# Optimization experiments

Measured on AMD Instinct MI355X. Metric: run time of the kernel, lower is better.

Reference implementation:

```python
import jax, jax.numpy as jnp
import numpy as np

N = 4096      # num_nodes (unbatched seq len for the transformer)
D = 128       # input_dim = window = d_model
H = 4         # num_heads
DH = D // H
DFF = 2048    # PyTorch TransformerEncoderLayer default dim_feedforward
HID = 256     # hidden_dim
OUT = 64      # output_dim
E = 131072    # num_edges (avg degree 32)
EPS = 1e-5    # LayerNorm eps (torch default)


def layer_norm(x, g, b):
    mu = jnp.mean(x, axis=-1, keepdims=True)
    var = jnp.var(x, axis=-1, keepdims=True)
    return (x - mu) * jax.lax.rsqrt(var + EPS) * g + b


def gcn_conv(x, W, b, src, dst):
    # PyG GCNConv: h = x W^T; add self-loops; symmetric deg^-1/2 norm; scatter-add at dst; + bias
    h = x @ W.T
    loop = jnp.arange(N)
    s = jnp.concatenate([src, loop])
    t = jnp.concatenate([dst, loop])
    deg = jax.ops.segment_sum(jnp.ones_like(t, dtype=h.dtype), t, num_segments=N)
    dinv = jnp.where(deg > 0, jax.lax.rsqrt(jnp.maximum(deg, 1e-12)), 0.0)
    norm = dinv[s] * dinv[t]                                   # [E+N]
    out = jax.ops.segment_sum(h[s] * norm[:, None], t, num_segments=N)
    return out + b


def setup_inputs() -> dict:
    key = jax.random.key(0)
    ks = jax.random.split(key, 12)
    sc = 0.05
    w = lambda k, shape: jax.random.normal(k, shape, dtype=jnp.float32) * sc
    return {
        "x": jax.random.normal(ks[0], (N, D), dtype=jnp.float32),
        "edge_index": jax.random.randint(ks[1], (2, E), 0, N),
        "in_proj_w": w(ks[2], (3 * D, D)),
        "in_proj_b": jnp.zeros((3 * D,), jnp.float32),
        "out_proj_w": w(ks[3], (D, D)),
        "out_proj_b": jnp.zeros((D,), jnp.float32),
        "ln1_g": jnp.ones((D,), jnp.float32),
        "ln1_b": jnp.zeros((D,), jnp.float32),
        "ffn_w1": w(ks[4], (DFF, D)),
        "ffn_b1": jnp.zeros((DFF,), jnp.float32),
        "ffn_w2": w(ks[5], (D, DFF)),
        "ffn_b2": jnp.zeros((D,), jnp.float32),
        "ln2_g": jnp.ones((D,), jnp.float32),
        "ln2_b": jnp.zeros((D,), jnp.float32),
        "gcn1_w": w(ks[6], (HID, D)),
        "gcn1_b": jnp.zeros((HID,), jnp.float32),
        "gcn2_w": w(ks[7], (HID, HID)),
        "gcn2_b": jnp.zeros((HID,), jnp.float32),
        "gcn3_w": w(ks[8], (OUT, HID)),
        "gcn3_b": jnp.zeros((OUT,), jnp.float32),
    }


def reference(x, edge_index, in_proj_w, in_proj_b, out_proj_w, out_proj_b,
              ln1_g, ln1_b, ffn_w1, ffn_b1, ffn_w2, ffn_b2, ln2_g, ln2_b,
              gcn1_w, gcn1_b, gcn2_w, gcn2_b, gcn3_w, gcn3_b):
    src, dst = edge_index[0], edge_index[1]
    # --- TransformerEncoderLayer (post-norm, relu, dropout=0, unbatched [N, D]) ---
    qkv = x @ in_proj_w.T + in_proj_b
    q, k, v = jnp.split(qkv, 3, axis=-1)
    q = q.reshape(N, H, DH)
    k = k.reshape(N, H, DH)
    v = v.reshape(N, H, DH)
    scores = jnp.einsum('nhd,mhd->hnm', q, k) / jnp.sqrt(jnp.float32(DH))
    attn = jax.nn.softmax(scores, axis=-1)
    ctx = jnp.einsum('hnm,mhd->nhd', attn, v).reshape(N, D)
    attn_out = ctx @ out_proj_w.T + out_proj_b
    y = layer_norm(x + attn_out, ln1_g, ln1_b)
    ff = jax.nn.relu(y @ ffn_w1.T + ffn_b1) @ ffn_w2.T + ffn_b2
    z = layer_norm(y + ff, ln2_g, ln2_b)
    # x.squeeze(-1) is a no-op since window (=128) > 1
    # --- 3-layer GCN with ReLU between layers ---
    h = jax.nn.relu(gcn_conv(z, gcn1_w, gcn1_b, src, dst))
    h = jax.nn.relu(gcn_conv(h, gcn2_w, gcn2_b, src, dst))
    return gcn_conv(h, gcn3_w, gcn3_b, src, dst)
```

## Files before the change

kernel.cpp:

```cpp
#include <hip/hip_runtime.h>


typedef unsigned short u16;
typedef __attribute__((ext_vector_type(8))) short bf16x8;
typedef __attribute__((ext_vector_type(4))) float f32x4;

__device__ __forceinline__ float b2f(u16 u) {
  union { unsigned int i; float f; } x; x.i = ((unsigned int)u) << 16; return x.f;
}
__device__ __forceinline__ u16 f2b(float f) {
  union { float f; unsigned int i; } x; x.f = f;
  unsigned int r = x.i + 0x7FFFu + ((x.i >> 16) & 1u);
  return (u16)(r >> 16);
}
__device__ __forceinline__ float ld1(const void* p, size_t i, int bf) {
  return bf ? b2f(((const u16*)p)[i]) : ((const float*)p)[i];
}

__device__ void gemm_body(
    int bx, int by, int bz, int nz,
    const void* __restrict__ A, const void* __restrict__ B,
    const void* __restrict__ bias, void* __restrict__ C, void* __restrict__ C2,
    int N, int K, int lda, int ldb, int bRow0, int bK0, int flags,
    const int* __restrict__ dflag, const float* __restrict__ divL)
{
  const int wbf = *dflag;
  const int abf = (flags & 64) ? 0 : ((flags & 16) ? wbf : 1);
  __shared__ u16 As[64][128];
  __shared__ u16 Bs[64][128];
  const int tid = threadIdx.x;
  const int wv = tid >> 6, l = tid & 63;
  const int lr = l & 15, lq = l >> 4;
  const int row0 = by * 64, col0 = bx * 64;
  const int qr = 32 * (wv >> 1), qc = 32 * (wv & 1);
  const int sr = tid >> 2, sb = tid & 3;
  const int Kz = K / nz;
  const int k0 = bz * Kz;
  f32x4 acc[2][2] = {};
  for (int kt = k0; kt < k0 + Kz; kt += 128) {
    __syncthreads();
#pragma unroll
    for (int g = 0; g < 4; g++) {
      int b = sb + 4 * g;
      int cc = b * 8;
      int bs = (b ^ (sr & 15)) * 8;
      size_t offA = (size_t)(row0 + sr) * lda + kt + cc;
      if (abf) {
        *(bf16x8*)&As[sr][bs] = *(const bf16x8*)((const u16*)A + offA);
      } else {
        const float* pf = (const float*)A + offA;
        float iv = divL
            ? 1.0f / divL[(size_t)((kt + cc) >> 5) * 4096 + row0 + sr]
            : 1.0f;
        float4 f0 = *(const float4*)pf, f1 = *(const float4*)(pf + 4);
        u16 t[8] = {f2b(f0.x*iv), f2b(f0.y*iv), f2b(f0.z*iv), f2b(f0.w*iv),
                    f2b(f1.x*iv), f2b(f1.y*iv), f2b(f1.z*iv), f2b(f1.w*iv)};
        *(bf16x8*)&As[sr][bs] = *(bf16x8*)t;
      }
      size_t offB = (size_t)(bRow0 + col0 + sr) * ldb + bK0 + kt + cc;
      if (wbf) {
        *(bf16x8*)&Bs[sr][bs] = *(const bf16x8*)((const u16*)B + offB);
      } else {
        const float* pf = (const float*)B + offB;
        float4 f0 = *(const float4*)pf, f1 = *(const float4*)(pf + 4);
        u16 t[8] = {f2b(f0.x), f2b(f0.y), f2b(f0.z), f2b(f0.w),
                    f2b(f1.x), f2b(f1.y), f2b(f1.z), f2b(f1.w)};
        *(bf16x8*)&Bs[sr][bs] = *(bf16x8*)t;
      }
    }
    __syncthreads();
#pragma unroll
    for (int kk = 0; kk < 4; kk++) {
      int bxs = ((4 * kk + lq) ^ lr) * 8;
      bf16x8 a0 = *(const bf16x8*)&As[qr + lr][bxs];
      bf16x8 a1 = *(const bf16x8*)&As[qr + 16 + lr][bxs];
      bf16x8 b0 = *(const bf16x8*)&Bs[qc + lr][bxs];
      bf16x8 b1 = *(const bf16x8*)&Bs[qc + 16 + lr][bxs];
      acc[0][0] = __builtin_amdgcn_mfma_f32_16x16x32_bf16(a0, b0, acc[0][0], 0, 0, 0);
      acc[0][1] = __builtin_amdgcn_mfma_f32_16x16x32_bf16(a0, b1, acc[0][1], 0, 0, 0);
      acc[1][0] = __builtin_amdgcn_mfma_f32_16x16x32_bf16(a1, b0, acc[1][0], 0, 0, 0);
      acc[1][1] = __builtin_amdgcn_mfma_f32_16x16x32_bf16(a1, b1, acc[1][1], 0, 0, 0);
    }
  }
  if ((flags & 128) && col0 >= 256) {
#pragma unroll
    for (int i = 0; i < 2; i++) {
#pragma unroll
      for (int j = 0; j < 2; j++) {
        int colg = col0 + qc + 16 * j + lr;
        int d = colg - 256;
        int rowbase = row0 + qr + 16 * i + lq * 4;
        float bb = ld1(bias, colg, wbf);
        ushort4 pv = make_ushort4(
            f2b(acc[i][j][0] + bb), f2b(acc[i][j][1] + bb),
            f2b(acc[i][j][2] + bb), f2b(acc[i][j][3] + bb));
        *(ushort4*)((u16*)C2 + (size_t)d * 4096 + rowbase) = pv;
      }
    }
    return;
  }
  const int ldc = (flags & 128) ? 256 : N;
#pragma unroll
  for (int i = 0; i < 2; i++) {
#pragma unroll
    for (int j = 0; j < 2; j++) {
#pragma unroll
      for (int r = 0; r < 4; r++) {
        int row = row0 + qr + 16 * i + lq * 4 + r;
        int col = col0 + qc + 16 * j + lr;
        float v = acc[i][j][r];
        if (flags & 8) v += ld1(bias, bRow0 + col, wbf);
        if (flags & 1) v = fmaxf(v, 0.f);
        size_t idx = (size_t)row * ldc + col;
        if (flags & 32) {
          atomicAdd(&((float*)C)[idx], v);
        } else if (flags & 4) {
          float* Cf = (float*)C;
          if (flags & 2) v += Cf[idx];
          Cf[idx] = v;
        } else {
          ((u16*)C)[idx] = f2b(v);
        }
      }
    }
  }
}

__global__ __launch_bounds__(256) void gemm_mfma(
    const void* __restrict__ A, const void* __restrict__ B,
    const void* __restrict__ bias, void* __restrict__ C, void* __restrict__ C2,
    int N, int K, int lda, int ldb, int bRow0, int bK0, int flags,
    const int* __restrict__ dflag, const float* __restrict__ divL)
{
  gemm_body(blockIdx.x, blockIdx.y, blockIdx.z, gridDim.z,
            A, B, bias, C, C2, N, K, lda, ldb, bRow0, bK0, flags, dflag, divL);
}

__global__ __launch_bounds__(256) void det_count(
    const void* __restrict__ x, int* __restrict__ flag,
    const int* __restrict__ dst, int* __restrict__ counts, int E)
{
  if (blockIdx.x == 0) {
    __shared__ int cnt;
    if (threadIdx.x == 0) cnt = 0;
    __syncthreads();
    const u16* p = (const u16*)x;
    int c = 0;
    for (int i = threadIdx.x; i < 4096; i += 256) {
      int e = (p[i] >> 7) & 0xFF;
      if (e >= 140) c++;
    }
    atomicAdd(&cnt, c);
    __syncthreads();
    if (threadIdx.x == 0) flag[0] = (cnt < 64) ? 1 : 0;
  } else {
    int e = (blockIdx.x - 1) * 256 + threadIdx.x;
    if (e < E) atomicAdd(&counts[dst[e]], 1);
  }
}

__global__ __launch_bounds__(256) void csr_inproj(
    const void* __restrict__ xin, const void* __restrict__ W,
    const void* __restrict__ bias, void* __restrict__ qkQK, void* __restrict__ Vg,
    const int* __restrict__ dflag,
    const int* __restrict__ src, const int* __restrict__ dst,
    const int* __restrict__ offs, int* __restrict__ cursor,
    int* __restrict__ csr, int E)
{
  if (blockIdx.x < 384) {
    gemm_body(blockIdx.x % 6, blockIdx.x / 6, 0, 1,
              xin, W, bias, qkQK, Vg, 384, 128, 128, 128, 0, 0,
               8 | 16 | 128, dflag, nullptr);
  } else {
    int e = (blockIdx.x - 384) * 256 + threadIdx.x;
    if (e < E) {
      int t = dst[e];
      int pos = offs[t] + atomicAdd(&cursor[t], 1);
      csr[pos] = src[e];
    }
  }
}

__global__ __launch_bounds__(256) void attn_part(
    const u16* __restrict__ qk, const u16* __restrict__ Vg,
    float* __restrict__ O, float* __restrict__ L)
{
  const int qt = blockIdx.x, h = blockIdx.y, kc = blockIdx.z;
  const int n0 = qt * 64;
  __shared__ u16 Qs[64][32];
  __shared__ u16 Ks[128][32];
  __shared__ u16 Vt[32][128];
  __shared__ u16 Ps[64][128];
  const int tid = threadIdx.x;
  const int wv = tid >> 6, l = tid & 63;
  const int lr = l & 15, lq = l >> 4;
  const int sr = tid >> 2, sb = tid & 3;
  const int kr = tid >> 1, kb = tid & 1;
  const int vr = tid >> 3, vb = tid & 7;
  *(bf16x8*)&Qs[sr][(sb ^ (sr & 3)) * 8] =
      *(const bf16x8*)(qk + (size_t)(n0 + sr) * 256 + h * 32 + sb * 8);
  __syncthreads();
  const float sc = 0.17677669529663687f;
  bf16x8 qf;
  {
    bf16x8 qraw = *(const bf16x8*)&Qs[16 * wv + lr][(lq ^ (lr & 3)) * 8];
#pragma unroll
    for (int t = 0; t < 8; t++)
      qf[t] = (short)f2b(b2f((u16)qraw[t]) * sc);
  }
  f32x4 o0 = {}, o1 = {};
  float psum[4] = {0.f, 0.f, 0.f, 0.f};
  for (int t = 0; t < 8; t++) {
    const int m0 = kc * 1024 + t * 128;
    __syncthreads();
#pragma unroll
    for (int cc = 0; cc < 2; cc++) {
      int ch = kb + 2 * cc;
      *(bf16x8*)&Ks[kr][(ch ^ (kr & 3)) * 8] =
          *(const bf16x8*)(qk + (size_t)(m0 + kr) * 256 + 128 + h * 32 + ch * 8);
    }
#pragma unroll
    for (int cc = 0; cc < 2; cc++) {
      int ch = vb + 8 * cc;
      *(bf16x8*)&Vt[vr][(ch ^ (vr & 15)) * 8] =
          *(const bf16x8*)(Vg + (size_t)(h * 32 + vr) * 4096 + m0 + ch * 8);
    }
    __syncthreads();
    f32x4 s[8];
#pragma unroll
    for (int jt = 0; jt < 8; jt++) {
      bf16x8 kf = *(const bf16x8*)&Ks[16 * jt + lr][(lq ^ (lr & 3)) * 8];
      f32x4 z = {};
      s[jt] = __builtin_amdgcn_mfma_f32_16x16x32_bf16(qf, kf, z, 0, 0, 0);
    }
#pragma unroll
    for (int jt = 0; jt < 8; jt++)
#pragma unroll
      for (int r = 0; r < 4; r++) {
        float p = __expf(s[jt][r]);
        psum[r] += p;
        int qrow = 16 * wv + lq * 4 + r;
        int ch = 2 * jt + (lr >> 3);
        Ps[qrow][(ch ^ (qrow & 15)) * 8 + (lr & 7)] = f2b(p);
      }
    __syncthreads();
#pragma unroll
    for (int kk = 0; kk < 4; kk++) {
      int prow = 16 * wv + lr;
      bf16x8 pf = *(const bf16x8*)&Ps[prow][((4 * kk + lq) ^ (lr & 15)) * 8];
      bf16x8 v0 = *(const bf16x8*)&Vt[lr][((4 * kk + lq) ^ (lr & 15)) * 8];
      bf16x8 v1 = *(const bf16x8*)&Vt[16 + lr][((4 * kk + lq) ^ (lr & 15)) * 8];
      o0 = __builtin_amdgcn_mfma_f32_16x16x32_bf16(pf, v0, o0, 0, 0, 0);
      o1 = __builtin_amdgcn_mfma_f32_16x16x32_bf16(pf, v1, o1, 0, 0, 0);
    }
  }
#pragma unroll
  for (int r = 0; r < 4; r++) {
    int row = n0 + 16 * wv + lq * 4 + r;
    atomicAdd(&O[(size_t)row * 128 + h * 32 + lr],      o0[r]);
    atomicAdd(&O[(size_t)row * 128 + h * 32 + 16 + lr], o1[r]);
    float ps = psum[r];
    ps += __shfl_xor(ps, 1); ps += __shfl_xor(ps, 2);
    ps += __shfl_xor(ps, 4); ps += __shfl_xor(ps, 8);
    if (lr == 0) atomicAdd(&L[h * 4096 + row], ps);
  }
}

__global__ __launch_bounds__(256) void ln_res(
    const void* __restrict__ A, int a_mode, const float* __restrict__ R,
    const void* __restrict__ rbias,
    const void* __restrict__ g, const void* __restrict__ b,
    u16* __restrict__ out_bf, float* __restrict__ out_f32,
    const int* __restrict__ dflag)
{
  const int wbf = *dflag;
  const int abf = a_mode ? wbf : 0;
  int row = blockIdx.x * 4 + (threadIdx.x >> 6);
  int lane = threadIdx.x & 63;
  size_t i0 = (size_t)row * 128 + lane, i1 = i0 + 64;
  float v0 = ld1(A, i0, abf) + R[i0];
  float v1 = ld1(A, i1, abf) + R[i1];
  if (rbias) { v0 += ld1(rbias, lane, wbf); v1 += ld1(rbias, lane + 64, wbf); }
  float s = v0 + v1, sq = v0 * v0 + v1 * v1;
  for (int off = 32; off; off >>= 1) { s += __shfl_down(s, off); sq += __shfl_down(sq, off); }
  s = __shfl(s, 0); sq = __shfl(sq, 0);
  float mu = s * (1.f / 128.f);
  float var = sq * (1.f / 128.f) - mu * mu;
  float rs = rsqrtf(var + 1e-5f);
  float r0 = (v0 - mu) * rs * ld1(g, lane, wbf) + ld1(b, lane, wbf);
  float r1 = (v1 - mu) * rs * ld1(g, lane + 64, wbf) + ld1(b, lane + 64, wbf);
  out_bf[i0] = f2b(r0);
  out_bf[i1] = f2b(r1);
  if (out_f32) { out_f32[i0] = r0; out_f32[i1] = r1; }
}

__global__ __launch_bounds__(1024) void scan4096(
    const int* __restrict__ counts, int* __restrict__ offs,
    float* __restrict__ dinv)
{
  __shared__ int buf[4096];
  __shared__ int part[1024];
  int t = threadIdx.x;
  for (int i = t; i < 4096; i += 1024) buf[i] = counts[i];
  __syncthreads();
  int base = t * 4;
  int s = buf[base] + buf[base + 1] + buf[base + 2] + buf[base + 3];
  part[t] = s;
  __syncthreads();
  for (int off = 1; off < 1024; off <<= 1) {
    int v = (t >= off) ? part[t - off] : 0;
    __syncthreads();
    part[t] += v;
    __syncthreads();
  }
  int run = (t == 0) ? 0 : part[t - 1];
  for (int j = 0; j < 4; j++) {
    int c = buf[base + j];
    offs[base + j] = run;
    dinv[base + j] = rsqrtf((float)(c + 1));
    run += c;
  }
  if (t == 1023) offs[4096] = run;
}

__global__ __launch_bounds__(256) void gcn_gather(
    const u16* __restrict__ h, const float* __restrict__ dinv,
    const int* __restrict__ offs, const int* __restrict__ csr,
    const void* __restrict__ bias, void* __restrict__ out,
    int F, int relu, int final_out, const int* __restrict__ dflag)
{
  const int wbf = *dflag;
  const int tpn = F >> 2;
  const int node = blockIdx.x * (256 / tpn) + threadIdx.x / tpn;
  const int f = (threadIdx.x % tpn) * 4;
  float di = dinv[node];
  ushort4 hv = *(const ushort4*)(h + (size_t)node * F + f);
  float a0 = di * b2f(hv.x), a1 = di * b2f(hv.y);
  float a2 = di * b2f(hv.z), a3 = di * b2f(hv.w);
  int e0 = offs[node], e1 = offs[node + 1];
  for (int e = e0; e < e1; e++) {
    int s = csr[e];
    float ds = dinv[s];
    ushort4 sv = *(const ushort4*)(h + (size_t)s * F + f);
    a0 += ds * b2f(sv.x); a1 += ds * b2f(sv.y);
    a2 += ds * b2f(sv.z); a3 += ds * b2f(sv.w);
  }
  float b0 = bias ? ld1(bias, f, wbf)     : 0.f;
  float b1 = bias ? ld1(bias, f + 1, wbf) : 0.f;
  float b2 = bias ? ld1(bias, f + 2, wbf) : 0.f;
  float b3 = bias ? ld1(bias, f + 3, wbf) : 0.f;
  float v0 = a0 * di + b0, v1 = a1 * di + b1;
  float v2 = a2 * di + b2, v3 = a3 * di + b3;
  if (relu) {
    v0 = fmaxf(v0, 0.f); v1 = fmaxf(v1, 0.f);
    v2 = fmaxf(v2, 0.f); v3 = fmaxf(v3, 0.f);
  }
  size_t idx = (size_t)node * F + f;
  if (!final_out || wbf) {
    *(ushort4*)((u16*)out + idx) = make_ushort4(f2b(v0), f2b(v1), f2b(v2), f2b(v3));
  } else {
    *(float4*)((float*)out + idx) = make_float4(v0, v1, v2, v3);
  }
}

extern "C" void kernel_launch(void* const* d_in, const int* in_sizes, int n_in,
                              void* d_out, int out_size, void* d_ws, size_t ws_size,
                              hipStream_t stream)
{
  const void* x          = d_in[0];
  const int*  edge       = (const int*)d_in[1];
  const void* in_proj_w  = d_in[2];
  const void* in_proj_b  = d_in[3];
  const void* out_proj_w = d_in[4];
  const void* out_proj_b = d_in[5];
  const void* ln1_g      = d_in[6];
  const void* ln1_b      = d_in[7];
  const void* ffn_w1     = d_in[8];
  const void* ffn_b1     = d_in[9];
  const void* ffn_w2     = d_in[10];
  const void* ffn_b2     = d_in[11];
  const void* ln2_g      = d_in[12];
  const void* ln2_b      = d_in[13];
  const void* g1w        = d_in[14];
  const void* g1b        = d_in[15];
  const void* g2w        = d_in[16];
  const void* g2b        = d_in[17];
  const void* g3w        = d_in[18];
  const void* g3b        = d_in[19];
  const int E = in_sizes[1] / 2;
  const int* esrc = edge;
  const int* edst = edge + E;

  char* wsb     = (char*)d_ws;
  u16*   qkQK   = (u16*)(wsb + 0);
  u16*   Vg     = (u16*)(wsb + 2097152);
  float* Oacc   = (float*)(wsb + 3145728);
  float* Lacc   = (float*)(wsb + 5242880);
  float* ff2    = (float*)(wsb + 5308416);
  int*   counts = (int*)(wsb + 7405568);
  int*   cursor = (int*)(wsb + 7421952);
  int*   offs   = (int*)(wsb + 7438336);
  int*   csr    = (int*)(wsb + 7454724);
  float* dinv   = (float*)(wsb + 7979012);
  int*   dflag  = (int*)(wsb + 7995396);
  float* y_f32  = (float*)(wsb + 8388608);
  u16*   y_bf   = (u16*)(wsb + 10485760);
  float* ao     = (float*)(wsb + 11534336);
  u16*   z_bf   = (u16*)(wsb + 13631488);
  u16*   az     = (u16*)(wsb + 14680064);
  u16*   h1     = (u16*)(wsb + 15728640);
  u16*   ah1    = (u16*)(wsb + 17825792);
  u16*   h2     = (u16*)(wsb + 19922944);
  u16*   t3     = (u16*)(wsb + 22020096);
  u16*   ff1    = (u16*)(wsb + 23068672);

  hipMemsetAsync(wsb + 3145728, 0, 4292608, stream);
  det_count<<<513, 256, 0, stream>>>(x, dflag, edst, counts, E);
  scan4096<<<1, 1024, 0, stream>>>(counts, offs, dinv);
  csr_inproj<<<896, 256, 0, stream>>>(x, in_proj_w, in_proj_b, qkQK, Vg, dflag,
      esrc, edst, offs, cursor, csr, E);

  attn_part<<<dim3(64, 4, 4), 256, 0, stream>>>(qkQK, Vg, Oacc, Lacc);
  gemm_mfma<<<dim3(2, 64), 256, 0, stream>>>(Oacc, out_proj_w, out_proj_b, ao, nullptr,
      128, 128, 128, 128, 0, 0,  4 | 8 | 64, dflag, Lacc);
  ln_res<<<1024, 256, 0, stream>>>(x, 1, ao, nullptr, ln1_g, ln1_b, y_bf, y_f32, dflag);
  gemm_mfma<<<dim3(32, 64), 256, 0, stream>>>(y_bf, ffn_w1, ffn_b1, ff1, nullptr,
      2048, 128, 128, 128, 0, 0,  1 | 8, dflag, nullptr);
  gemm_mfma<<<dim3(2, 64, 8), 256, 0, stream>>>(ff1, ffn_w2, nullptr, ff2, nullptr,
      128, 2048, 2048, 2048, 0, 0,  4 | 32, dflag, nullptr);
  ln_res<<<1024, 256, 0, stream>>>(y_f32, 0, ff2, ffn_b2, ln2_g, ln2_b, z_bf, nullptr, dflag);

  gcn_gather<<<512, 256, 0, stream>>>(z_bf, dinv, offs, csr, nullptr, az, 128, 0, 0, dflag);
  gemm_mfma<<<dim3(4, 64), 256, 0, stream>>>(az, g1w, g1b, h1, nullptr,
      256, 128, 128, 128, 0, 0,  1 | 8, dflag, nullptr);
  gcn_gather<<<1024, 256, 0, stream>>>(h1, dinv, offs, csr, nullptr, ah1, 256, 0, 0, dflag);
  gemm_mfma<<<dim3(4, 64), 256, 0, stream>>>(ah1, g2w, g2b, h2, nullptr,
      256, 256, 256, 256, 0, 0,  1 | 8, dflag, nullptr);
  gemm_mfma<<<dim3(1, 64), 256, 0, stream>>>(h2, g3w, nullptr, t3, nullptr,
      64, 256, 256, 256, 0, 0, 0, dflag, nullptr);
  gcn_gather<<<256, 256, 0, stream>>>(t3, dinv, offs, csr, g3b, d_out, 64, 0, 1, dflag);
}
```

Before: 295.4 us.

## Replace atomics with split-K partial buffers, fuse out-proj+LN, vectorize gathers, warp-scan

Attention and FFN2 split-K partial results are now written to separate per-chunk buffers instead of accumulated with float atomics, which removes most of the large workspace memset. The out-projection GEMM, softmax normalization, residual add and LayerNorm are fused into one oproj_ln kernel, and ln_res sums the FFN2 partials itself. GCN gathers use 8-wide bf16 loads with two threads per node splitting the edges, and the degree scan uses wave shuffles instead of a shared-memory Hillis-Steele loop. The cost is more workspace memory and extra partial-buffer reads in the reducing kernels.

```diff
diff --git a/kernel.cpp b/kernel.cpp
--- a/kernel.cpp
+++ b/kernel.cpp
@@ -113,7 +113,7 @@
         if (flags & 1) v = fmaxf(v, 0.f);
         size_t idx = (size_t)row * ldc + col;
         if (flags & 32) {
-          atomicAdd(&((float*)C)[idx], v);
+          ((float*)C)[(size_t)bz * 524288 + idx] = v;
         } else if (flags & 4) {
           float* Cf = (float*)C;
           if (flags & 2) v += Cf[idx];
@@ -254,21 +254,115 @@
       o1 = __builtin_amdgcn_mfma_f32_16x16x32_bf16(pf, v1, o1, 0, 0, 0);
     }
   }
+  const size_t ko = (size_t)kc * 524288;
+  float* Lk = L + (size_t)kc * 16384;
 #pragma unroll
   for (int r = 0; r < 4; r++) {
     int row = n0 + 16 * wv + lq * 4 + r;
-    atomicAdd(&O[(size_t)row * 128 + h * 32 + lr],      o0[r]);
-    atomicAdd(&O[(size_t)row * 128 + h * 32 + 16 + lr], o1[r]);
+    O[ko + (size_t)row * 128 + h * 32 + lr]      = o0[r];
+    O[ko + (size_t)row * 128 + h * 32 + 16 + lr] = o1[r];
     float ps = psum[r];
     ps += __shfl_xor(ps, 1); ps += __shfl_xor(ps, 2);
     ps += __shfl_xor(ps, 4); ps += __shfl_xor(ps, 8);
-    if (lr == 0) atomicAdd(&L[h * 4096 + row], ps);
+    if (lr == 0) Lk[h * 4096 + row] = ps;
+  }
+}
+
+__global__ __launch_bounds__(256) void oproj_ln(
+    const float* __restrict__ Op, const float* __restrict__ Lp,
+    const void* __restrict__ W, const void* __restrict__ bias,
+    const void* __restrict__ x, const void* __restrict__ g,
+    const void* __restrict__ bln, u16* __restrict__ y_bf,
+    float* __restrict__ y_f32, const int* __restrict__ dflag)
+{
+  const int wbf = *dflag;
+  __shared__ u16 As[16][128];
+  __shared__ u16 Bs[128][128];
+  const int tid = threadIdx.x;
+  const int r0 = blockIdx.x * 16;
+  {
+    int r = tid >> 4, b = tid & 15;
+    int hh = b >> 2;
+    float Ls = Lp[hh * 4096 + r0 + r] + Lp[16384 + hh * 4096 + r0 + r]
+             + Lp[32768 + hh * 4096 + r0 + r] + Lp[49152 + hh * 4096 + r0 + r];
+    float iv = 1.0f / Ls;
+    float a8[8] = {};
+#pragma unroll
+    for (int kc = 0; kc < 4; kc++) {
+      const float* p = Op + (size_t)kc * 524288 + (size_t)(r0 + r) * 128 + b * 8;
+      float4 q0 = *(const float4*)p, q1 = *(const float4*)(p + 4);
+      a8[0] += q0.x; a8[1] += q0.y; a8[2] += q0.z; a8[3] += q0.w;
+      a8[4] += q1.x; a8[5] += q1.y; a8[6] += q1.z; a8[7] += q1.w;
+    }
+    u16 t[8];
+#pragma unroll
+    for (int j = 0; j < 8; j++) t[j] = f2b(a8[j] * iv);
+    *(bf16x8*)&As[r][(b ^ r) * 8] = *(bf16x8*)t;
+  }
+  {
+    int o = tid >> 1, half = tid & 1;
+#pragma unroll
+    for (int bb8 = 0; bb8 < 8; bb8++) {
+      int b = half * 8 + bb8;
+      size_t off = (size_t)o * 128 + b * 8;
+      if (wbf) {
+        *(bf16x8*)&Bs[o][(b ^ (o & 15)) * 8] = *(const bf16x8*)((const u16*)W + off);
+      } else {
+        const float* pf = (const float*)W + off;
+        float4 f0 = *(const float4*)pf, f1 = *(const float4*)(pf + 4);
+        u16 t[8] = {f2b(f0.x), f2b(f0.y), f2b(f0.z), f2b(f0.w),
+                    f2b(f1.x), f2b(f1.y), f2b(f1.z), f2b(f1.w)};
+        *(bf16x8*)&Bs[o][(b ^ (o & 15)) * 8] = *(bf16x8*)t;
+      }
+    }
+  }
+  __syncthreads();
+  const int wv = tid >> 6, l = tid & 63;
+  const int lr = l & 15, lq = l >> 4;
+  const int c0 = 32 * wv;
+  f32x4 acc[2] = {};
+#pragma unroll
+  for (int kk = 0; kk < 4; kk++) {
+    int bxs = ((4 * kk + lq) ^ lr) * 8;
+    bf16x8 a0 = *(const bf16x8*)&As[lr][bxs];
+    bf16x8 b0 = *(const bf16x8*)&Bs[c0 + lr][bxs];
+    bf16x8 b1 = *(const bf16x8*)&Bs[c0 + 16 + lr][bxs];
+    acc[0] = __builtin_amdgcn_mfma_f32_16x16x32_bf16(a0, b0, acc[0], 0, 0, 0);
+    acc[1] = __builtin_amdgcn_mfma_f32_16x16x32_bf16(a0, b1, acc[1], 0, 0, 0);
+  }
+  __syncthreads();
+  float* Cf = (float*)&Bs[0][0];
+#pragma unroll
+  for (int j = 0; j < 2; j++)
+#pragma unroll
+    for (int r = 0; r < 4; r++) {
+      int row = lq * 4 + r, col = c0 + 16 * j + lr;
+      float v = acc[j][r] + ld1(bias, col, wbf)
+              + ld1(x, (size_t)(r0 + row) * 128 + col, wbf);
+      Cf[row * 128 + col] = v;
+    }
+  __syncthreads();
+#pragma unroll
+  for (int it = 0; it < 4; it++) {
+    int row = it * 4 + wv;
+    float v0 = Cf[row * 128 + l], v1 = Cf[row * 128 + 64 + l];
+    float s = v0 + v1, sq = v0 * v0 + v1 * v1;
+    for (int off = 32; off; off >>= 1) { s += __shfl_down(s, off); sq += __shfl_down(sq, off); }
+    s = __shfl(s, 0); sq = __shfl(sq, 0);
+    float mu = s * (1.f / 128.f);
+    float var = sq * (1.f / 128.f) - mu * mu;
+    float rs = rsqrtf(var + 1e-5f);
+    float o0 = (v0 - mu) * rs * ld1(g, l, wbf) + ld1(bln, l, wbf);
+    float o1 = (v1 - mu) * rs * ld1(g, l + 64, wbf) + ld1(bln, l + 64, wbf);
+    size_t i0 = (size_t)(r0 + row) * 128 + l;
+    y_bf[i0] = f2b(o0); y_bf[i0 + 64] = f2b(o1);
+    y_f32[i0] = o0; y_f32[i0 + 64] = o1;
   }
 }
 
 __global__ __launch_bounds__(256) void ln_res(
     const void* __restrict__ A, int a_mode, const float* __restrict__ R,
-    const void* __restrict__ rbias,
+    int nacc, const void* __restrict__ rbias,
     const void* __restrict__ g, const void* __restrict__ b,
     u16* __restrict__ out_bf, float* __restrict__ out_f32,
     const int* __restrict__ dflag)
@@ -278,8 +372,13 @@
   int row = blockIdx.x * 4 + (threadIdx.x >> 6);
   int lane = threadIdx.x & 63;
   size_t i0 = (size_t)row * 128 + lane, i1 = i0 + 64;
-  float v0 = ld1(A, i0, abf) + R[i0];
-  float v1 = ld1(A, i1, abf) + R[i1];
+  float r0a = 0.f, r1a = 0.f;
+  for (int z = 0; z < nacc; z++) {
+    r0a += R[(size_t)z * 524288 + i0];
+    r1a += R[(size_t)z * 524288 + i1];
+  }
+  float v0 = ld1(A, i0, abf) + r0a;
+  float v1 = ld1(A, i1, abf) + r1a;
   if (rbias) { v0 += ld1(rbias, lane, wbf); v1 += ld1(rbias, lane + 64, wbf); }
   float s = v0 + v1, sq = v0 * v0 + v1 * v1;
   for (int off = 32; off; off >>= 1) { s += __shfl_down(s, off); sq += __shfl_down(sq, off); }
@@ -298,29 +397,71 @@
     const int* __restrict__ counts, int* __restrict__ offs,
     float* __restrict__ dinv)
 {
-  __shared__ int buf[4096];
-  __shared__ int part[1024];
+  __shared__ int wsum[16];
   int t = threadIdx.x;
-  for (int i = t; i < 4096; i += 1024) buf[i] = counts[i];
+  int lane = t & 63, wid = t >> 6;
+  int4 c4 = *(const int4*)(counts + t * 4);
+  int own = c4.x + c4.y + c4.z + c4.w;
+  int s = own;
+  for (int off = 1; off < 64; off <<= 1) {
+    int n = __shfl_up(s, off);
+    if (lane >= off) s += n;
+  }
+  if (lane == 63) wsum[wid] = s;
   __syncthreads();
+  if (wid == 0) {
+    int w = (lane < 16) ? wsum[lane] : 0;
+    for (int off = 1; off < 16; off <<= 1) {
+      int n = __shfl_up(w, off);
+      if (lane >= off) w += n;
+    }
+    if (lane < 16) wsum[lane] = w;
+  }
+  __syncthreads();
+  int run = (wid ? wsum[wid - 1] : 0) + s - own;
   int base = t * 4;
-  int s = buf[base] + buf[base + 1] + buf[base + 2] + buf[base + 3];
-  part[t] = s;
-  __syncthreads();
-  for (int off = 1; off < 1024; off <<= 1) {
-    int v = (t >= off) ? part[t - off] : 0;
-    __syncthreads();
-    part[t] += v;
-    __syncthreads();
-  }
-  int run = (t == 0) ? 0 : part[t - 1];
+  int cv[4] = {c4.x, c4.y, c4.z, c4.w};
+#pragma unroll
   for (int j = 0; j < 4; j++) {
-    int c = buf[base + j];
     offs[base + j] = run;
-    dinv[base + j] = rsqrtf((float)(c + 1));
-    run += c;
+    dinv[base + j] = rsqrtf((float)(cv[j] + 1));
+    run += cv[j];
   }
   if (t == 1023) offs[4096] = run;
+}
+
+__global__ __launch_bounds__(256) void gcn_gather8(
+    const u16* __restrict__ h, const float* __restrict__ dinv,
+    const int* __restrict__ offs, const int* __restrict__ csr,
+    u16* __restrict__ out, int F)
+{
+  const int ft = F >> 3;
+  const int tpn = ft << 1;
+  const int node = blockIdx.x * (256 / tpn) + threadIdx.x / tpn;
+  const int sub = (threadIdx.x % tpn) / ft;
+  const int f = (threadIdx.x % ft) * 8;
+  float di = dinv[node];
+  float a[8] = {};
+  if (sub == 0) {
+    bf16x8 hv = *(const bf16x8*)(h + (size_t)node * F + f);
+#pragma unroll
+    for (int j = 0; j < 8; j++) a[j] = di * b2f((u16)hv[j]);
+  }
+  int e0 = offs[node], e1 = offs[node + 1];
+  for (int e = e0 + sub; e < e1; e += 2) {
+    int s = csr[e];
+    float ds = dinv[s];
+    bf16x8 sv = *(const bf16x8*)(h + (size_t)s * F + f);
+#pragma unroll
+    for (int j = 0; j < 8; j++) a[j] += ds * b2f((u16)sv[j]);
+  }
+#pragma unroll
+  for (int j = 0; j < 8; j++) a[j] += __shfl_xor(a[j], ft);
+  if (sub) return;
+  u16 t[8];
+#pragma unroll
+  for (int j = 0; j < 8; j++) t[j] = f2b(a[j] * di);
+  *(bf16x8*)(out + (size_t)node * F + f) = *(bf16x8*)t;
 }
 
 __global__ __launch_bounds__(256) void gcn_gather(
@@ -394,46 +535,45 @@
   char* wsb     = (char*)d_ws;
   u16*   qkQK   = (u16*)(wsb + 0);
   u16*   Vg     = (u16*)(wsb + 2097152);
-  float* Oacc   = (float*)(wsb + 3145728);
-  float* Lacc   = (float*)(wsb + 5242880);
-  float* ff2    = (float*)(wsb + 5308416);
-  int*   counts = (int*)(wsb + 7405568);
-  int*   cursor = (int*)(wsb + 7421952);
-  int*   offs   = (int*)(wsb + 7438336);
-  int*   csr    = (int*)(wsb + 7454724);
-  float* dinv   = (float*)(wsb + 7979012);
-  int*   dflag  = (int*)(wsb + 7995396);
-  float* y_f32  = (float*)(wsb + 8388608);
-  u16*   y_bf   = (u16*)(wsb + 10485760);
-  float* ao     = (float*)(wsb + 11534336);
-  u16*   z_bf   = (u16*)(wsb + 13631488);
-  u16*   az     = (u16*)(wsb + 14680064);
-  u16*   h1     = (u16*)(wsb + 15728640);
-  u16*   ah1    = (u16*)(wsb + 17825792);
-  u16*   h2     = (u16*)(wsb + 19922944);
-  u16*   t3     = (u16*)(wsb + 22020096);
-  u16*   ff1    = (u16*)(wsb + 23068672);
-
-  hipMemsetAsync(wsb + 3145728, 0, 4292608, stream);
+  float* Op     = (float*)(wsb + 3145728);
+  float* Lp     = (float*)(wsb + 11534336);
+  int*   counts = (int*)(wsb + 11796480);
+  int*   cursor = (int*)(wsb + 11812864);
+  int*   offs   = (int*)(wsb + 11829248);
+  int*   csr    = (int*)(wsb + 11845636);
+  float* dinv   = (float*)(wsb + 12369924);
+  int*   dflag  = (int*)(wsb + 12386308);
+  float* y_f32  = (float*)(wsb + 12582912);
+  u16*   y_bf   = (u16*)(wsb + 14680064);
+  u16*   z_bf   = (u16*)(wsb + 15728640);
+  u16*   az     = (u16*)(wsb + 16777216);
+  u16*   h1     = (u16*)(wsb + 17825792);
+  u16*   ah1    = (u16*)(wsb + 19922944);
+  u16*   h2     = (u16*)(wsb + 22020096);
+  u16*   t3     = (u16*)(wsb + 24117248);
+  u16*   ff1    = (u16*)(wsb + 25165824);
+  float* ff2p   = (float*)(wsb + 41943040);
+
+  hipMemsetAsync(wsb + 11796480, 0, 32768, stream);
   det_count<<<513, 256, 0, stream>>>(x, dflag, edst, counts, E);
   scan4096<<<1, 1024, 0, stream>>>(counts, offs, dinv);
   csr_inproj<<<896, 256, 0, stream>>>(x, in_proj_w, in_proj_b, qkQK, Vg, dflag,
       esrc, edst, offs, cursor, csr, E);
 
-  attn_part<<<dim3(64, 4, 4), 256, 0, stream>>>(qkQK, Vg, Oacc, Lacc);
-  gemm_mfma<<<dim3(2, 64), 256, 0, stream>>>(Oacc, out_proj_w, out_proj_b, ao, nullptr,
-      128, 128, 128, 128, 0, 0,  4 | 8 | 64, dflag, Lacc);
-  ln_res<<<1024, 256, 0, stream>>>(x, 1, ao, nullptr, ln1_g, ln1_b, y_bf, y_f32, dflag);
+  attn_part<<<dim3(64, 4, 4), 256, 0, stream>>>(qkQK, Vg, Op, Lp);
+  oproj_ln<<<256, 256, 0, stream>>>(Op, Lp, out_proj_w, out_proj_b, x,
+      ln1_g, ln1_b, y_bf, y_f32, dflag);
   gemm_mfma<<<dim3(32, 64), 256, 0, stream>>>(y_bf, ffn_w1, ffn_b1, ff1, nullptr,
       2048, 128, 128, 128, 0, 0,  1 | 8, dflag, nullptr);
-  gemm_mfma<<<dim3(2, 64, 8), 256, 0, stream>>>(ff1, ffn_w2, nullptr, ff2, nullptr,
-      128, 2048, 2048, 2048, 0, 0,  4 | 32, dflag, nullptr);
-  ln_res<<<1024, 256, 0, stream>>>(y_f32, 0, ff2, ffn_b2, ln2_g, ln2_b, z_bf, nullptr, dflag);
-
-  gcn_gather<<<512, 256, 0, stream>>>(z_bf, dinv, offs, csr, nullptr, az, 128, 0, 0, dflag);
+  gemm_mfma<<<dim3(2, 64, 8), 256, 0, stream>>>(ff1, ffn_w2, nullptr, ff2p, nullptr,
+      128, 2048, 2048, 2048, 0, 0,  32, dflag, nullptr);
+  ln_res<<<1024, 256, 0, stream>>>(y_f32, 0, ff2p, 8, ffn_b2, ln2_g, ln2_b,
+      z_bf, nullptr, dflag);
+
+  gcn_gather8<<<512, 256, 0, stream>>>(z_bf, dinv, offs, csr, az, 128);
   gemm_mfma<<<dim3(4, 64), 256, 0, stream>>>(az, g1w, g1b, h1, nullptr,
       256, 128, 128, 128, 0, 0,  1 | 8, dflag, nullptr);
-  gcn_gather<<<1024, 256, 0, stream>>>(h1, dinv, offs, csr, nullptr, ah1, 256, 0, 0, dflag);
+  gcn_gather8<<<1024, 256, 0, stream>>>(h1, dinv, offs, csr, ah1, 256);
   gemm_mfma<<<dim3(4, 64), 256, 0, stream>>>(ah1, g2w, g2b, h2, nullptr,
       256, 256, 256, 256, 0, 0,  1 | 8, dflag, nullptr);
   gemm_mfma<<<dim3(1, 64), 256, 0, stream>>>(h2, g3w, nullptr, t3, nullptr,
```

New measurement: 269.3 us. -8.8%, faster.
